# Optimization experiments

Measured on AMD Instinct MI355X. Metric: run time of the kernel, lower is better.

## Reference

```python
import jax, jax.numpy as jnp
import numpy as np

NUM_LABELS = 500  # labels 0..499; 0 = background (excluded)

def setup_inputs() -> dict:
    key = jax.random.key(0)
    k1, k2 = jax.random.split(key)
    x = jax.random.normal(k1, (8, 3, 1024, 1024), dtype=jnp.float32)
    target = jax.random.randint(k2, (8, 1024, 1024), 0, NUM_LABELS, dtype=jnp.int32)
    return {"x": x, "target": target}

def reference(x, target):
    # Faithful to LossVariance: per sample, per nonzero label, take the [C, n]
    # pixel gather and add torch.var over ALL C*n elements (unbiased), skipping
    # instances with n <= 1; normalize by (#unique nonzero labels + 1e-8); mean over batch.
    B, C, H, W = x.shape
    L = NUM_LABELS
    P = H * W
    xf = x.reshape(B, C, P)
    seg = (target.reshape(B, P) + jnp.arange(B, dtype=target.dtype)[:, None] * L).reshape(-1)
    # per-pixel channel-reduced sums -> segmented sums over (batch, label)
    s = jax.ops.segment_sum(xf.sum(axis=1).reshape(-1), seg, num_segments=B * L).reshape(B, L)
    ss = jax.ops.segment_sum((xf * xf).sum(axis=1).reshape(-1), seg, num_segments=B * L).reshape(B, L)
    cnt = jax.ops.segment_sum(jnp.ones((B * P,), dtype=x.dtype), seg, num_segments=B * L).reshape(B, L)
    # drop background label 0
    s, ss, cnt = s[:, 1:], ss[:, 1:], cnt[:, 1:]
    N = C * cnt                       # total elements in the [C, n] gather
    valid = cnt > 1                   # original skips instances with n <= 1
    safe_N = jnp.where(cnt > 0, N, 1.0)
    safe_den = jnp.where(valid, N - 1.0, 1.0)
    var = jnp.where(valid, (ss - s * s / safe_N) / safe_den, 0.0)  # unbiased var over C*n elems
    n_unique = (cnt > 0).sum(axis=1).astype(x.dtype)               # nonzero labels present
    loss_per_sample = var.sum(axis=1) / (n_unique + 1e-8)
    return loss_per_sample.mean()
```

## Files before the change

### kernel.cpp

```cpp
#include <hip/hip_runtime.h>

#define NUM_LABELS 500
#define NB 8
#define NP (1024 * 1024)
#define BPB 128
#define TPB 512


__device__ __forceinline__ void lv_accum(unsigned long long* h, int t,
                                         float a, float b, float c) {
    if (t > 0) {
        float v = a + b + c;
        float q = a * a + b * b + c * c;
        unsigned vf = (unsigned)(fmaf(v, 256.f, 16384.5f));
        unsigned qf = (unsigned)(fmaf(q, 64.f, 0.5f));
        unsigned long long pk =
            (1ULL << 48) | ((unsigned long long)vf << 24) | (unsigned long long)qf;
        atomicAdd(&h[t], pk);
    }
}

__global__ __launch_bounds__(TPB) void lv_bins(const float* __restrict__ x,
                                               const int* __restrict__ tgt,
                                               float* __restrict__ bins) {
    __shared__ unsigned long long h[NUM_LABELS];

    const int b = blockIdx.y;
    for (int i = threadIdx.x; i < NUM_LABELS; i += TPB) h[i] = 0ULL;
    __syncthreads();

    const float* x0 = x + (size_t)(b * 3 + 0) * NP;
    const float* x1 = x + (size_t)(b * 3 + 1) * NP;
    const float* x2 = x + (size_t)(b * 3 + 2) * NP;
    const int*   tg = tgt + (size_t)b * NP;

    const int pixPerBlock = NP / BPB;
    const int stride = TPB * 4;
    const int nIter = pixPerBlock / stride;

    int p = blockIdx.x * pixPerBlock + (int)threadIdx.x * 4;

    int4   t4 = *(const int4*)(tg + p);
    float4 a4 = *(const float4*)(x0 + p);
    float4 b4 = *(const float4*)(x1 + p);
    float4 c4 = *(const float4*)(x2 + p);

    for (int it = 0; it < nIter - 1; ++it) {
        const int pn = p + stride;
        int4   tn = *(const int4*)(tg + pn);
        float4 an = *(const float4*)(x0 + pn);
        float4 bn = *(const float4*)(x1 + pn);
        float4 cn = *(const float4*)(x2 + pn);

        lv_accum(h, t4.x, a4.x, b4.x, c4.x);
        lv_accum(h, t4.y, a4.y, b4.y, c4.y);
        lv_accum(h, t4.z, a4.z, b4.z, c4.z);
        lv_accum(h, t4.w, a4.w, b4.w, c4.w);

        t4 = tn; a4 = an; b4 = bn; c4 = cn;
        p = pn;
    }
    lv_accum(h, t4.x, a4.x, b4.x, c4.x);
    lv_accum(h, t4.y, a4.y, b4.y, c4.y);
    lv_accum(h, t4.z, a4.z, b4.z, c4.z);
    lv_accum(h, t4.w, a4.w, b4.w, c4.w);

    __syncthreads();

    float* g_s = bins;
    float* g_q = bins + NB * NUM_LABELS;
    float* g_c = bins + 2 * NB * NUM_LABELS;
    for (int i = threadIdx.x; i < NUM_LABELS; i += TPB) {
        unsigned long long w = h[i];
        if (w != 0ULL) {
            float cnt = (float)(unsigned)(w >> 48);
            float sv  = (float)(unsigned)((w >> 24) & 0xFFFFFFu) * (1.f / 256.f)
                        - 64.f * cnt;
            float sq  = (float)(unsigned)(w & 0xFFFFFFu) * (1.f / 64.f);
            atomicAdd(&g_s[b * NUM_LABELS + i], sv);
            atomicAdd(&g_q[b * NUM_LABELS + i], sq);
            atomicAdd(&g_c[b * NUM_LABELS + i], cnt);
        }
    }
}

__global__ __launch_bounds__(512) void lv_final(const float* __restrict__ bins,
                                                float* __restrict__ out) {
    const int wave = threadIdx.x >> 6;
    const int lane = threadIdx.x & 63;

    const float* g_s = bins;
    const float* g_q = bins + NB * NUM_LABELS;
    const float* g_c = bins + 2 * NB * NUM_LABELS;

    float var_sum = 0.f;
    float uniq = 0.f;
    for (int l = 1 + lane; l < NUM_LABELS; l += 64) {
        float c = g_c[wave * NUM_LABELS + l];
        float s = g_s[wave * NUM_LABELS + l];
        float q = g_q[wave * NUM_LABELS + l];
        if (c > 0.f) uniq += 1.f;
        if (c > 1.f) {
            float N = 3.f * c;
            var_sum += (q - s * s / N) / (N - 1.f);
        }
    }
    for (int off = 32; off > 0; off >>= 1) {
        var_sum += __shfl_down(var_sum, off);
        uniq    += __shfl_down(uniq, off);
    }

    __shared__ float part[NB];
    if (lane == 0) part[wave] = var_sum / (uniq + 1e-8f);
    __syncthreads();

    if (threadIdx.x == 0) {
        float acc = 0.f;
        for (int i = 0; i < NB; ++i) acc += part[i];
        out[0] = acc * (1.f / NB);
    }
}

extern "C" void kernel_launch(void* const* d_in, const int* in_sizes, int n_in,
                              void* d_out, int out_size, void* d_ws, size_t ws_size,
                              hipStream_t stream) {
    const float* x   = (const float*)d_in[0];
    const int*   tgt = (const int*)d_in[1];
    float*       out = (float*)d_out;
    float*       bins = (float*)d_ws;

    hipMemsetAsync(bins, 0, (size_t)3 * NB * NUM_LABELS * sizeof(float), stream);

    dim3 grid(BPB, NB);
    lv_bins<<<grid, TPB, 0, stream>>>(x, tgt, bins);
    lv_final<<<1, 512, 0, stream>>>(bins, out);
}
```

Before: 178.1 us.

## Fuse final reduction via last-block counter, duplicate shared histograms, halve block count

Drops the separate finalize kernel: a global atomic counter elects the last block, which then computes the variance loss in double precision. Each block keeps two shared histograms selected by thread parity to cut LDS atomic contention. Global accumulation switches from three float atomics to two packed 64-bit integer atomics, and blocks per batch are halved. This saves a launch and some global atomic traffic, at the cost of fewer blocks in flight and a serialized tail in the last block.

New measurement: 302.2 us. 69.6% more time.

```diff
diff --git a/kernel.cpp b/kernel.cpp
--- a/kernel.cpp
+++ b/kernel.cpp
@@ -3,11 +3,12 @@
 #define NUM_LABELS 500
 #define NB 8
 #define NP (1024 * 1024)
-#define BPB 128
+#define BPB 64
 #define TPB 512
+#define NBLK (BPB * NB)
 
 
-__device__ __forceinline__ void lv_accum(unsigned long long* h, int t,
+__device__ __forceinline__ void lv_accum(unsigned long long* hc, int t,
                                          float a, float b, float c) {
     if (t > 0) {
         float v = a + b + c;
@@ -16,18 +17,23 @@
         unsigned qf = (unsigned)(fmaf(q, 64.f, 0.5f));
         unsigned long long pk =
             (1ULL << 48) | ((unsigned long long)vf << 24) | (unsigned long long)qf;
-        atomicAdd(&h[t], pk);
+        atomicAdd(&hc[t], pk);
     }
 }
 
 __global__ __launch_bounds__(TPB) void lv_bins(const float* __restrict__ x,
                                                const int* __restrict__ tgt,
-                                               float* __restrict__ bins) {
-    __shared__ unsigned long long h[NUM_LABELS];
+                                               unsigned long long* __restrict__ g1,
+                                               unsigned long long* __restrict__ g2,
+                                               unsigned int* __restrict__ counter,
+                                               float* __restrict__ out) {
+    __shared__ unsigned long long hist[2 * NUM_LABELS];
 
     const int b = blockIdx.y;
-    for (int i = threadIdx.x; i < NUM_LABELS; i += TPB) h[i] = 0ULL;
+    for (int i = threadIdx.x; i < 2 * NUM_LABELS; i += TPB) hist[i] = 0ULL;
     __syncthreads();
+
+    unsigned long long* hc = hist + (threadIdx.x & 1) * NUM_LABELS;
 
     const float* x0 = x + (size_t)(b * 3 + 0) * NP;
     const float* x1 = x + (size_t)(b * 3 + 1) * NP;
@@ -52,57 +58,58 @@
         float4 bn = *(const float4*)(x1 + pn);
         float4 cn = *(const float4*)(x2 + pn);
 
-        lv_accum(h, t4.x, a4.x, b4.x, c4.x);
-        lv_accum(h, t4.y, a4.y, b4.y, c4.y);
-        lv_accum(h, t4.z, a4.z, b4.z, c4.z);
-        lv_accum(h, t4.w, a4.w, b4.w, c4.w);
+        lv_accum(hc, t4.x, a4.x, b4.x, c4.x);
+        lv_accum(hc, t4.y, a4.y, b4.y, c4.y);
+        lv_accum(hc, t4.z, a4.z, b4.z, c4.z);
+        lv_accum(hc, t4.w, a4.w, b4.w, c4.w);
 
         t4 = tn; a4 = an; b4 = bn; c4 = cn;
         p = pn;
     }
-    lv_accum(h, t4.x, a4.x, b4.x, c4.x);
-    lv_accum(h, t4.y, a4.y, b4.y, c4.y);
-    lv_accum(h, t4.z, a4.z, b4.z, c4.z);
-    lv_accum(h, t4.w, a4.w, b4.w, c4.w);
+    lv_accum(hc, t4.x, a4.x, b4.x, c4.x);
+    lv_accum(hc, t4.y, a4.y, b4.y, c4.y);
+    lv_accum(hc, t4.z, a4.z, b4.z, c4.z);
+    lv_accum(hc, t4.w, a4.w, b4.w, c4.w);
 
     __syncthreads();
 
-    float* g_s = bins;
-    float* g_q = bins + NB * NUM_LABELS;
-    float* g_c = bins + 2 * NB * NUM_LABELS;
     for (int i = threadIdx.x; i < NUM_LABELS; i += TPB) {
-        unsigned long long w = h[i];
+        unsigned long long w = hist[i] + hist[NUM_LABELS + i];
         if (w != 0ULL) {
-            float cnt = (float)(unsigned)(w >> 48);
-            float sv  = (float)(unsigned)((w >> 24) & 0xFFFFFFu) * (1.f / 256.f)
-                        - 64.f * cnt;
-            float sq  = (float)(unsigned)(w & 0xFFFFFFu) * (1.f / 64.f);
-            atomicAdd(&g_s[b * NUM_LABELS + i], sv);
-            atomicAdd(&g_q[b * NUM_LABELS + i], sq);
-            atomicAdd(&g_c[b * NUM_LABELS + i], cnt);
+            unsigned long long cnt = w >> 48;
+            unsigned long long vf  = (w >> 24) & 0xFFFFFFULL;
+            unsigned long long qf  = w & 0xFFFFFFULL;
+            atomicAdd(&g1[b * NUM_LABELS + i], (cnt << 32) | vf);
+            atomicAdd(&g2[b * NUM_LABELS + i], qf);
         }
     }
-}
 
-__global__ __launch_bounds__(512) void lv_final(const float* __restrict__ bins,
-                                                float* __restrict__ out) {
-    const int wave = threadIdx.x >> 6;
+    __threadfence();
+    __shared__ int lastFlag;
+    if (threadIdx.x == 0) {
+        unsigned int old = __hip_atomic_fetch_add(counter, 1u, __ATOMIC_ACQ_REL,
+                                                  __HIP_MEMORY_SCOPE_AGENT);
+        lastFlag = (old == (unsigned)(NBLK - 1)) ? 1 : 0;
+    }
+    __syncthreads();
+    if (!lastFlag) return;
+
+    const int wv   = threadIdx.x >> 6;
     const int lane = threadIdx.x & 63;
 
-    const float* g_s = bins;
-    const float* g_q = bins + NB * NUM_LABELS;
-    const float* g_c = bins + 2 * NB * NUM_LABELS;
-
-    float var_sum = 0.f;
-    float uniq = 0.f;
+    double var_sum = 0.0, uniq = 0.0;
     for (int l = 1 + lane; l < NUM_LABELS; l += 64) {
-        float c = g_c[wave * NUM_LABELS + l];
-        float s = g_s[wave * NUM_LABELS + l];
-        float q = g_q[wave * NUM_LABELS + l];
-        if (c > 0.f) uniq += 1.f;
-        if (c > 1.f) {
-            float N = 3.f * c;
-            var_sum += (q - s * s / N) / (N - 1.f);
+        unsigned long long a1 = __hip_atomic_load(&g1[wv * NUM_LABELS + l],
+                                                  __ATOMIC_RELAXED, __HIP_MEMORY_SCOPE_AGENT);
+        unsigned long long a2 = __hip_atomic_load(&g2[wv * NUM_LABELS + l],
+                                                  __ATOMIC_RELAXED, __HIP_MEMORY_SCOPE_AGENT);
+        double cnt = (double)(a1 >> 32);
+        double sv  = (double)(a1 & 0xFFFFFFFFULL) * (1.0 / 256.0) - 64.0 * cnt;
+        double sq  = (double)a2 * (1.0 / 64.0);
+        if (cnt > 0.0) uniq += 1.0;
+        if (cnt > 1.0) {
+            double N = 3.0 * cnt;
+            var_sum += (sq - sv * sv / N) / (N - 1.0);
         }
     }
     for (int off = 32; off > 0; off >>= 1) {
@@ -110,14 +117,14 @@
         uniq    += __shfl_down(uniq, off);
     }
 
-    __shared__ float part[NB];
-    if (lane == 0) part[wave] = var_sum / (uniq + 1e-8f);
+    __shared__ double part[NB];
+    if (lane == 0) part[wv] = var_sum / (uniq + 1e-8);
     __syncthreads();
 
     if (threadIdx.x == 0) {
-        float acc = 0.f;
+        double acc = 0.0;
         for (int i = 0; i < NB; ++i) acc += part[i];
-        out[0] = acc * (1.f / NB);
+        out[0] = (float)(acc * (1.0 / NB));
     }
 }
 
@@ -127,11 +134,13 @@
     const float* x   = (const float*)d_in[0];
     const int*   tgt = (const int*)d_in[1];
     float*       out = (float*)d_out;
-    float*       bins = (float*)d_ws;
 
-    hipMemsetAsync(bins, 0, (size_t)3 * NB * NUM_LABELS * sizeof(float), stream);
+    unsigned long long* g1 = (unsigned long long*)d_ws;
+    unsigned long long* g2 = g1 + NB * NUM_LABELS;
+    unsigned int* counter  = (unsigned int*)(g2 + NB * NUM_LABELS);
+
+    hipMemsetAsync(d_ws, 0, (size_t)NB * NUM_LABELS * 16 + 64, stream);
 
     dim3 grid(BPB, NB);
-    lv_bins<<<grid, TPB, 0, stream>>>(x, tgt, bins);
-    lv_final<<<1, 512, 0, stream>>>(bins, out);
+    lv_bins<<<grid, TPB, 0, stream>>>(x, tgt, g1, g2, counter, out);
 }
```
